# Optimization experiments

Hardware: AMD Instinct MI355X
Metric: run time of the kernel (lower is better)

Reference implementation:

```python
import jax, jax.numpy as jnp
import numpy as np

N_NODES = 100000
N_EDGES = 1600000
NODE_F = 64
EDGE_F = 32
BN_EPS = 1e-5


def setup_inputs() -> dict:
    key = jax.random.key(0)
    ks = jax.random.split(key, 8)
    in_dim = 2 * NODE_F + EDGE_F  # 160
    scale = 1.0 / np.sqrt(in_dim)
    return {
        "node_attrs": jax.random.normal(ks[0], (N_NODES, NODE_F), jnp.float32),
        "edge_index": jax.random.randint(ks[1], (2, N_EDGES), 0, N_NODES, jnp.int64),
        "edge_attrs": jax.random.normal(ks[2], (N_EDGES, EDGE_F), jnp.float32),
        "W_f": jax.random.normal(ks[3], (in_dim, NODE_F), jnp.float32) * scale,
        "b_f": jnp.zeros((NODE_F,), jnp.float32),
        "W_s": jax.random.normal(ks[4], (in_dim, NODE_F), jnp.float32) * scale,
        "b_s": jnp.zeros((NODE_F,), jnp.float32),
        "gamma": jnp.ones((NODE_F,), jnp.float32),
        "beta": jnp.zeros((NODE_F,), jnp.float32),
    }


def reference(node_attrs, edge_index, edge_attrs, W_f, b_f, W_s, b_s, gamma, beta):
    source, target = edge_index[0], edge_index[1]
    x_i = node_attrs[source]            # [E, F] gather
    x_j = node_attrs[target]            # [E, F] gather
    z = jnp.concatenate([x_i, x_j, edge_attrs], axis=-1)  # [E, 2F+Fe]
    # gated MLP: sigmoid(lin_f(z)) * softplus(lin_s(z))
    h = jax.nn.sigmoid(z @ W_f + b_f) * jax.nn.softplus(z @ W_s + b_s)  # [E, F]
    # scatter-add messages to source nodes
    message = jax.ops.segment_sum(h, source, num_segments=node_attrs.shape[0])  # [N, F]
    # BatchNorm1d in training mode: batch stats over node dim (biased variance)
    mean = jnp.mean(message, axis=0)
    var = jnp.mean((message - mean) ** 2, axis=0)
    normed = (message - mean) * jax.lax.rsqrt(var + BN_EPS) * gamma + beta
    return node_attrs + normed
```

## Files before the change

kernel.cpp:

```cpp
#include <hip/hip_runtime.h>
#include <math.h>

#define N_NODES 100000
#define N_EDGES 1600000
#define NODE_F  64
#define IN_DIM  160
#define N_TILES 25000
#define ZSTRIDE 168
#define EDGE_GRID 1536
#define PQ_GRID  2048
#define PRE_GRID 512
#define PRE_TILES 1563

typedef __attribute__((ext_vector_type(8))) short short8;
typedef __attribute__((ext_vector_type(4))) float f32x4;

static __device__ inline unsigned short f2bf(float f) {
    union { float f; unsigned u; } v; v.f = f;
    unsigned r = v.u + 0x7fffu + ((v.u >> 16) & 1u);
    return (unsigned short)(r >> 16);
}

static __device__ inline unsigned pack2(float lo, float hi) {
    union { float f; unsigned u; } a, b; a.f = lo; b.f = hi;
    const unsigned ra = a.u + 0x7fffu + ((a.u >> 16) & 1u);
    const unsigned rb = b.u + 0x7fffu + ((b.u >> 16) & 1u);
    return __builtin_amdgcn_perm(rb, ra, 0x07060302u);
}

__global__ __launch_bounds__(256, 3) void precompute_kernel(
    const float* __restrict__ X,
    const float* __restrict__ W_f, const float* __restrict__ W_s,
    float* __restrict__ PS, float* __restrict__ QT)
{
    __shared__ __align__(16) short wtps[128 * 68];
    __shared__ __align__(16) short wtqt[128 * 68];
    __shared__ __align__(16) short xl[64 * 72];
    unsigned* xl32 = (unsigned*)xl;

    const int tid  = threadIdx.x;
    const int wave = tid >> 6;
    const int lane = tid & 63;
    const int quad = lane >> 4;
    const int l15  = lane & 15;

    for (int idx = tid; idx < 128 * 64; idx += 256) {
        const int c = idx >> 6;
        const int k = idx & 63;
        const int j = c >> 1;
        const float* W = (c & 1) ? W_s : W_f;
        wtps[c * 68 + k] = (short)f2bf(W[k * 64 + j]);
        wtqt[c * 68 + k] = (short)f2bf(W[(k + 64) * 64 + j]);
    }
    __syncthreads();

    const short* wt = (wave >> 1) ? wtqt : wtps;
    const int colbase = (wave & 1) * 64;
    float* const OUT = (wave >> 1) ? QT : PS;

    short8 bfr[4][2];
#pragma unroll
    for (int nt = 0; nt < 4; ++nt)
#pragma unroll
        for (int kc = 0; kc < 2; ++kc)
            bfr[nt][kc] = *(const short8*)&wt[(colbase + nt * 16 + l15) * 68 + kc * 32 + quad * 8];

    for (int t = blockIdx.x; t < PRE_TILES; t += PRE_GRID) {
        const int n0 = t * 64;
        __syncthreads();
        for (int idx = tid; idx < 64 * 16; idx += 256) {
            const int row = idx >> 4, c4 = idx & 15;
            float4 v = {0.f, 0.f, 0.f, 0.f};
            if (n0 + row < N_NODES)
                v = *(const float4*)&X[(size_t)(n0 + row) * 64 + c4 * 4];
            uint2 o; o.x = pack2(v.x, v.y); o.y = pack2(v.z, v.w);
            *(uint2*)&xl32[row * 36 + c4 * 2] = o;
        }
        __syncthreads();

#pragma unroll
        for (int mt = 0; mt < 4; ++mt) {
            short8 a0 = *(const short8*)&xl[(mt * 16 + l15) * 72 + 0 * 32 + quad * 8];
            short8 a1 = *(const short8*)&xl[(mt * 16 + l15) * 72 + 1 * 32 + quad * 8];
#pragma unroll
            for (int nt = 0; nt < 4; ++nt) {
                f32x4 acc = {0.f, 0.f, 0.f, 0.f};
                acc = __builtin_amdgcn_mfma_f32_16x16x32_bf16(a0, bfr[nt][0], acc, 0, 0, 0);
                acc = __builtin_amdgcn_mfma_f32_16x16x32_bf16(a1, bfr[nt][1], acc, 0, 0, 0);
#pragma unroll
                for (int r = 0; r < 4; ++r) {
                    const int node = n0 + mt * 16 + quad * 4 + r;
                    if (node < N_NODES)
                        OUT[(size_t)node * 128 + colbase + nt * 16 + l15] = acc[r];
                }
            }
        }
    }
}

__global__ __launch_bounds__(256, 8) void edge_pq_kernel(
    const float* __restrict__ PS,
    const float* __restrict__ QT,
    const int*   __restrict__ edge_src,
    const int*   __restrict__ edge_tgt,
    const float* __restrict__ edge_attrs,
    const float* __restrict__ W_f, const float* __restrict__ b_f,
    const float* __restrict__ W_s, const float* __restrict__ b_s,
    float* __restrict__ msg)
{
    __shared__ __align__(16) short ebuf[64 * 40];
    __shared__ __align__(16) short wet[64 * 72];

    const int tid  = threadIdx.x;
    const int wave = tid >> 6;
    const int lane = tid & 63;
    const int quad = lane >> 4;
    const int l15  = lane & 15;

    for (int idx = tid; idx < 64 * 32; idx += 256) {
        const int c = idx >> 5, k = idx & 31;
        wet[c * 72 + k]      = (short)f2bf(W_f[(k + 128) * 64 + c]);
        wet[c * 72 + 32 + k] = (short)f2bf(W_s[(k + 128) * 64 + c]);
    }
    __syncthreads();
    const short8 bFe = *(const short8*)&wet[(16 * wave + l15) * 72 + quad * 8];
    const short8 bSe = *(const short8*)&wet[(16 * wave + l15) * 72 + 32 + quad * 8];

    const float bias_f = b_f[16 * wave + l15];
    const float bias_s = b_s[16 * wave + l15];
    const int   fcol2  = 2 * (16 * wave + l15);
    float* const msgf  = msg + 16 * wave + l15;

    const int sel = tid >> 2;
    const int sg  = tid & 3;

    int srcv = edge_src[blockIdx.x * 64 + lane];
    int tgtv = edge_tgt[blockIdx.x * 64 + lane];

    for (int t = blockIdx.x; t < N_TILES; t += PQ_GRID) {
        const int e0 = t * 64;

        __syncthreads();

        {
            const float4 v0 = *(const float4*)&edge_attrs[(size_t)(e0 + sel) * 32 + sg * 8];
            const float4 v1 = *(const float4*)&edge_attrs[(size_t)(e0 + sel) * 32 + sg * 8 + 4];
            short8 o;
            unsigned* o32 = (unsigned*)&o;
            o32[0] = pack2(v0.x, v0.y); o32[1] = pack2(v0.z, v0.w);
            o32[2] = pack2(v1.x, v1.y); o32[3] = pack2(v1.z, v1.w);
            *(short8*)&ebuf[sel * 40 + sg * 8] = o;
        }

        const int tn = t + PQ_GRID;
        int nsrc = 0, ntgt = 0;
        if (tn < N_TILES) {
            nsrc = edge_src[tn * 64 + lane];
            ntgt = edge_tgt[tn * 64 + lane];
        }
        __syncthreads();

#pragma unroll
        for (int mt = 0; mt < 4; ++mt) {
            const short8 a = *(const short8*)&ebuf[(mt * 16 + l15) * 40 + quad * 8];
            f32x4 accF = {0.f, 0.f, 0.f, 0.f};
            f32x4 accS = {0.f, 0.f, 0.f, 0.f};
            accF = __builtin_amdgcn_mfma_f32_16x16x32_bf16(a, bFe, accF, 0, 0, 0);
            accS = __builtin_amdgcn_mfma_f32_16x16x32_bf16(a, bSe, accS, 0, 0, 0);
#pragma unroll
            for (int r = 0; r < 4; ++r) {
                const int e = mt * 16 + quad * 4 + r;
                const int s = __shfl(srcv, e);
                const int g = __shfl(tgtv, e);
                const float2 ps = *(const float2*)&PS[(size_t)s * 128 + fcol2];
                const float2 qt = *(const float2*)&QT[(size_t)g * 128 + fcol2];
                const float xf = accF[r] + ps.x + qt.x + bias_f;
                const float xs = accS[r] + ps.y + qt.y + bias_s;
                const float sig = __builtin_amdgcn_rcpf(1.0f + __expf(-xf));
                const float sp  = fmaxf(xs, 0.0f) + __logf(1.0f + __expf(-fabsf(xs)));
                atomicAdd(&msgf[s * 64], sig * sp);
            }
        }

        srcv = nsrc;
        tgtv = ntgt;
    }
}

__global__ __launch_bounds__(256, 6) void edge_kernel(
    const float* __restrict__ node_attrs,
    const int*   __restrict__ edge_src,
    const int*   __restrict__ edge_tgt,
    const float* __restrict__ edge_attrs,
    const float* __restrict__ W_f, const float* __restrict__ b_f,
    const float* __restrict__ W_s, const float* __restrict__ b_s,
    float* __restrict__ msg)
{
    __shared__ __align__(16) short sbuf[64 * ZSTRIDE];
    unsigned* sbuf32 = (unsigned*)sbuf;

    const int tid  = threadIdx.x;
    const int wave = tid >> 6;
    const int lane = tid & 63;
    const int quad = lane >> 4;
    const int l15  = lane & 15;

    short8 bF[5], bS[5];
#pragma unroll
    for (int mat = 0; mat < 2; ++mat) {
        const float* W = mat ? W_s : W_f;
        __syncthreads();
        for (int idx = tid; idx < IN_DIM * 64; idx += 256) {
            const int k = idx >> 6, n = idx & 63;
            sbuf[n * ZSTRIDE + k] = (short)f2bf(W[idx]);
        }
        __syncthreads();
#pragma unroll
        for (int kc = 0; kc < 5; ++kc) {
            const short8 b = *(const short8*)&sbuf[(16 * wave + l15) * ZSTRIDE + kc * 32 + quad * 8];
            if (mat) bS[kc] = b; else bF[kc] = b;
        }
    }

    const float bias_f = b_f[16 * wave + l15];
    const float bias_s = b_s[16 * wave + l15];
    float* const msgf  = msg + 16 * wave + l15;

    int srcv = edge_src[blockIdx.x * 64 + lane];
    int tgtv = edge_tgt[blockIdx.x * 64 + lane];

    for (int t = blockIdx.x; t < N_TILES; t += EDGE_GRID) {
        const int e0 = t * 64;
        __syncthreads();
#pragma unroll
        for (int i = 0; i < 8; ++i) {
            const int el   = i * 2 + (quad >> 1);
            const int half = quad & 1;
            const int sl   = 16 * wave + el;
            const int ns   = __shfl(srcv, sl);
            const int nt   = __shfl(tgtv, sl);
            const int node = half ? nt : ns;
            const float4 v = *(const float4*)&node_attrs[node * 64 + l15 * 4];
            uint2 o; o.x = pack2(v.x, v.y); o.y = pack2(v.z, v.w);
            *(uint2*)&sbuf32[sl * (ZSTRIDE / 2) + half * 32 + l15 * 2] = o;
        }
#pragma unroll
        for (int i = 0; i < 2; ++i) {
            const int p  = i * 256 + tid;
            const int el = p >> 3, g = p & 7;
            const float4 v = *(const float4*)&edge_attrs[(size_t)(e0 + el) * 32 + g * 4];
            uint2 o; o.x = pack2(v.x, v.y); o.y = pack2(v.z, v.w);
            *(uint2*)&sbuf32[el * (ZSTRIDE / 2) + 64 + g * 2] = o;
        }
        const int tn = t + EDGE_GRID;
        int nsrc = 0, ntgt = 0;
        if (tn < N_TILES) {
            nsrc = edge_src[tn * 64 + lane];
            ntgt = edge_tgt[tn * 64 + lane];
        }
        __syncthreads();
#pragma unroll
        for (int mt = 0; mt < 4; ++mt) {
            f32x4 accF = {0.f, 0.f, 0.f, 0.f};
            f32x4 accS = {0.f, 0.f, 0.f, 0.f};
#pragma unroll
            for (int kc = 0; kc < 5; ++kc) {
                const short8 a = *(const short8*)&sbuf[(mt * 16 + l15) * ZSTRIDE + kc * 32 + quad * 8];
                accF = __builtin_amdgcn_mfma_f32_16x16x32_bf16(a, bF[kc], accF, 0, 0, 0);
                accS = __builtin_amdgcn_mfma_f32_16x16x32_bf16(a, bS[kc], accS, 0, 0, 0);
            }
#pragma unroll
            for (int r = 0; r < 4; ++r) {
                const float xf = accF[r] + bias_f;
                const float xs = accS[r] + bias_s;
                const float sig = __builtin_amdgcn_rcpf(1.0f + __expf(-xf));
                const float sp  = fmaxf(xs, 0.0f) + __logf(1.0f + __expf(-fabsf(xs)));
                const float h   = sig * sp;
                const int sl    = mt * 16 + quad * 4 + r;
                const int node  = __shfl(srcv, sl);
                atomicAdd(&msgf[node * 64], h);
            }
        }
        srcv = nsrc;
        tgtv = ntgt;
    }
}

#define STATS_BLOCKS 400
__global__ __launch_bounds__(256) void stats_kernel(
    const float* __restrict__ msg, float* __restrict__ stats)
{
    const int tid = threadIdx.x;
    const int f = tid & 63;
    const int g = tid >> 6;
    float s = 0.0f, q = 0.0f;
    for (int r = blockIdx.x * 4 + g; r < N_NODES; r += STATS_BLOCKS * 4) {
        const float v = msg[r * 64 + f];
        s += v;
        q = fmaf(v, v, q);
    }
    __shared__ float rs[4][64];
    __shared__ float rq[4][64];
    rs[g][f] = s;
    rq[g][f] = q;
    __syncthreads();
    if (tid < 64) {
        const float ss = rs[0][f] + rs[1][f] + rs[2][f] + rs[3][f];
        const float qq = rq[0][f] + rq[1][f] + rq[2][f] + rq[3][f];
        atomicAdd(&stats[f], ss);
        atomicAdd(&stats[64 + f], qq);
    }
}

__global__ __launch_bounds__(256) void norm_kernel(
    const float* __restrict__ node_attrs,
    const float* __restrict__ stats,
    const float* __restrict__ gamma,
    const float* __restrict__ beta,
    float* __restrict__ out)
{
    const int i = blockIdx.x * blockDim.x + threadIdx.x;
    const int idx = i * 4;
    if (idx >= N_NODES * 64) return;
    const int f = idx & 63;
    const float inv_n = 1.0f / (float)N_NODES;

    const float4 m4 = *(const float4*)&out[idx];
    const float4 x4 = *(const float4*)&node_attrs[idx];

    float mean[4], rstd[4], gm[4], bt[4];
#pragma unroll
    for (int j = 0; j < 4; ++j) {
        mean[j] = stats[f + j] * inv_n;
        const float var = stats[64 + f + j] * inv_n - mean[j] * mean[j];
        rstd[j] = rsqrtf(var + 1e-5f);
        gm[j] = gamma[f + j];
        bt[j] = beta[f + j];
    }
    float4 o;
    o.x = x4.x + (m4.x - mean[0]) * rstd[0] * gm[0] + bt[0];
    o.y = x4.y + (m4.y - mean[1]) * rstd[1] * gm[1] + bt[1];
    o.z = x4.z + (m4.z - mean[2]) * rstd[2] * gm[2] + bt[2];
    o.w = x4.w + (m4.w - mean[3]) * rstd[3] * gm[3] + bt[3];
    *(float4*)&out[idx] = o;
}

extern "C" void kernel_launch(void* const* d_in, const int* in_sizes, int n_in,
                              void* d_out, int out_size, void* d_ws, size_t ws_size,
                              hipStream_t stream)
{
    const float* node_attrs = (const float*)d_in[0];
    const int*   edge_index = (const int*)d_in[1];
    const float* edge_attrs = (const float*)d_in[2];
    const float* W_f   = (const float*)d_in[3];
    const float* b_f   = (const float*)d_in[4];
    const float* W_s   = (const float*)d_in[5];
    const float* b_s   = (const float*)d_in[6];
    const float* gamma = (const float*)d_in[7];
    const float* beta  = (const float*)d_in[8];

    float* out   = (float*)d_out;
    float* stats = (float*)d_ws;

    float* PS = (float*)((char*)d_ws + 4096);
    float* QT = PS + (size_t)N_NODES * 128;
    const size_t WS_NEED = 4096 + 2ull * N_NODES * 128 * sizeof(float);

    const int* edge_src = edge_index;
    const int* edge_tgt = edge_index + N_EDGES;

    hipMemsetAsync(out, 0, (size_t)N_NODES * NODE_F * sizeof(float), stream);
    hipMemsetAsync(stats, 0, 128 * sizeof(float), stream);

    if (ws_size >= WS_NEED) {
        precompute_kernel<<<PRE_GRID, 256, 0, stream>>>(node_attrs, W_f, W_s, PS, QT);
        edge_pq_kernel<<<PQ_GRID, 256, 0, stream>>>(
            PS, QT, edge_src, edge_tgt, edge_attrs, W_f, b_f, W_s, b_s, out);
    } else {
        edge_kernel<<<EDGE_GRID, 256, 0, stream>>>(
            node_attrs, edge_src, edge_tgt, edge_attrs, W_f, b_f, W_s, b_s, out);
    }

    stats_kernel<<<STATS_BLOCKS, 256, 0, stream>>>(out, stats);

    norm_kernel<<<(N_NODES * NODE_F / 4 + 255) / 256, 256, 0, stream>>>(
        node_attrs, stats, gamma, beta, out);
}
```

Measured before the change: 716.2 us.

## Sort edges by source node and aggregate messages per run before atomics

Adds a counting sort of edges by source (histogram, three-stage scan, fill and scatter kernels) so the edge kernel walks edges grouped by source node. Each lane accumulates consecutive same-source contributions in a register and issues one atomic per run, and loads the source's PS row only once per run. The goal is to cut global atomic traffic and redundant PS gathers. In exchange it adds several extra kernel launches with their own atomics and memory passes, and edge_attrs reads become indirect gathers through the permutation.

```diff
diff --git a/kernel.cpp b/kernel.cpp
--- a/kernel.cpp
+++ b/kernel.cpp
@@ -8,9 +8,11 @@
 #define N_TILES 25000
 #define ZSTRIDE 168
 #define EDGE_GRID 1536
-#define PQ_GRID  2048
+#define SPQ_GRID 2048
 #define PRE_GRID 512
 #define PRE_TILES 1563
+#define SCAN_BLOCKS 391
+#define E_BLOCKS    6250
 
 typedef __attribute__((ext_vector_type(8))) short short8;
 typedef __attribute__((ext_vector_type(4))) float f32x4;
@@ -26,6 +28,92 @@
     const unsigned ra = a.u + 0x7fffu + ((a.u >> 16) & 1u);
     const unsigned rb = b.u + 0x7fffu + ((b.u >> 16) & 1u);
     return __builtin_amdgcn_perm(rb, ra, 0x07060302u);
+}
+
+static __device__ inline int permrow(int e) {
+    return ((e >> 2) & 3) * 16 + (e >> 4) * 4 + (e & 3);
+}
+
+__global__ __launch_bounds__(256) void hist_kernel(
+    const int* __restrict__ src, int* __restrict__ hist)
+{
+    const int e = blockIdx.x * 256 + threadIdx.x;
+    if (e < N_EDGES) atomicAdd(&hist[src[e]], 1);
+}
+
+__global__ __launch_bounds__(256) void scan1_kernel(
+    const int* __restrict__ hist, int* __restrict__ partial)
+{
+    __shared__ int lds[256];
+    const int tid = threadIdx.x;
+    const int idx = blockIdx.x * 256 + tid;
+    lds[tid] = (idx < N_NODES) ? hist[idx] : 0;
+    __syncthreads();
+    for (int s = 128; s > 0; s >>= 1) {
+        if (tid < s) lds[tid] += lds[tid + s];
+        __syncthreads();
+    }
+    if (tid == 0) partial[blockIdx.x] = lds[0];
+}
+
+__global__ __launch_bounds__(512) void scan2_kernel(int* __restrict__ partial)
+{
+    __shared__ int lds[512];
+    const int tid = threadIdx.x;
+    const int v = (tid < SCAN_BLOCKS) ? partial[tid] : 0;
+    lds[tid] = v;
+    __syncthreads();
+    for (int off = 1; off < 512; off <<= 1) {
+        const int t = (tid >= off) ? lds[tid - off] : 0;
+        __syncthreads();
+        lds[tid] += t;
+        __syncthreads();
+    }
+    if (tid < SCAN_BLOCKS) partial[tid] = lds[tid] - v;
+}
+
+__global__ __launch_bounds__(256) void scan3_kernel(
+    const int* __restrict__ hist, const int* __restrict__ partial,
+    int* __restrict__ offs, int* __restrict__ cursor)
+{
+    __shared__ int lds[256];
+    const int tid = threadIdx.x;
+    const int idx = blockIdx.x * 256 + tid;
+    const int v = (idx < N_NODES) ? hist[idx] : 0;
+    lds[tid] = v;
+    __syncthreads();
+    for (int off = 1; off < 256; off <<= 1) {
+        const int t = (tid >= off) ? lds[tid - off] : 0;
+        __syncthreads();
+        lds[tid] += t;
+        __syncthreads();
+    }
+    if (idx < N_NODES) {
+        const int x = lds[tid] - v + partial[blockIdx.x];
+        offs[idx]   = x;
+        cursor[idx] = x;
+    }
+}
+
+__global__ __launch_bounds__(256) void fill_src_kernel(
+    const int* __restrict__ offs, int* __restrict__ sSrc)
+{
+    const int n = blockIdx.x * 256 + threadIdx.x;
+    if (n >= N_NODES) return;
+    const int s = offs[n];
+    const int e = (n + 1 < N_NODES) ? offs[n + 1] : N_EDGES;
+    for (int i = s; i < e; ++i) sSrc[i] = n;
+}
+
+__global__ __launch_bounds__(256) void scatter2_kernel(
+    const int* __restrict__ src, const int* __restrict__ tgt,
+    int* __restrict__ cursor, int2* __restrict__ tp)
+{
+    const int e = blockIdx.x * 256 + threadIdx.x;
+    if (e >= N_EDGES) return;
+    const int s = src[e];
+    const int pos = atomicAdd(&cursor[s], 1);
+    tp[pos] = make_int2(tgt[e], e);
 }
 
 __global__ __launch_bounds__(256, 3) void precompute_kernel(
@@ -98,11 +186,11 @@
     }
 }
 
-__global__ __launch_bounds__(256, 8) void edge_pq_kernel(
+__global__ __launch_bounds__(256, 8) void edge_sorted_pq_kernel(
     const float* __restrict__ PS,
     const float* __restrict__ QT,
-    const int*   __restrict__ edge_src,
-    const int*   __restrict__ edge_tgt,
+    const int*   __restrict__ sSrc,
+    const int2*  __restrict__ tp,
     const float* __restrict__ edge_attrs,
     const float* __restrict__ W_f, const float* __restrict__ b_f,
     const float* __restrict__ W_s, const float* __restrict__ b_s,
@@ -134,32 +222,34 @@
     const int sel = tid >> 2;
     const int sg  = tid & 3;
 
-    int srcv = edge_src[blockIdx.x * 64 + lane];
-    int tgtv = edge_tgt[blockIdx.x * 64 + lane];
-
-    for (int t = blockIdx.x; t < N_TILES; t += PQ_GRID) {
-        const int e0 = t * 64;
-
+    int  srcv = sSrc[blockIdx.x * 64 + lane];
+    int2 tpv  = tp[blockIdx.x * 64 + lane];
+
+    for (int t = blockIdx.x; t < N_TILES; t += SPQ_GRID) {
         __syncthreads();
 
         {
-            const float4 v0 = *(const float4*)&edge_attrs[(size_t)(e0 + sel) * 32 + sg * 8];
-            const float4 v1 = *(const float4*)&edge_attrs[(size_t)(e0 + sel) * 32 + sg * 8 + 4];
+            const int pe  = __shfl(tpv.y, sel);
+            const int row = permrow(sel);
+            const float4 v0 = *(const float4*)&edge_attrs[(size_t)pe * 32 + sg * 8];
+            const float4 v1 = *(const float4*)&edge_attrs[(size_t)pe * 32 + sg * 8 + 4];
             short8 o;
             unsigned* o32 = (unsigned*)&o;
             o32[0] = pack2(v0.x, v0.y); o32[1] = pack2(v0.z, v0.w);
             o32[2] = pack2(v1.x, v1.y); o32[3] = pack2(v1.z, v1.w);
-            *(short8*)&ebuf[sel * 40 + sg * 8] = o;
-        }
-
-        const int tn = t + PQ_GRID;
-        int nsrc = 0, ntgt = 0;
+            *(short8*)&ebuf[row * 40 + sg * 8] = o;
+        }
+
+        const int tn = t + SPQ_GRID;
+        int  nsrc = 0; int2 ntp = make_int2(0, 0);
         if (tn < N_TILES) {
-            nsrc = edge_src[tn * 64 + lane];
-            ntgt = edge_tgt[tn * 64 + lane];
-        }
-        __syncthreads();
-
+            nsrc = sSrc[tn * 64 + lane];
+            ntp  = tp[tn * 64 + lane];
+        }
+        __syncthreads();
+
+        int lastn = -1;
+        float carry = 0.0f, psx = 0.0f, psy = 0.0f;
 #pragma unroll
         for (int mt = 0; mt < 4; ++mt) {
             const short8 a = *(const short8*)&ebuf[(mt * 16 + l15) * 40 + quad * 8];
@@ -169,21 +259,27 @@
             accS = __builtin_amdgcn_mfma_f32_16x16x32_bf16(a, bSe, accS, 0, 0, 0);
 #pragma unroll
             for (int r = 0; r < 4; ++r) {
-                const int e = mt * 16 + quad * 4 + r;
-                const int s = __shfl(srcv, e);
-                const int g = __shfl(tgtv, e);
-                const float2 ps = *(const float2*)&PS[(size_t)s * 128 + fcol2];
-                const float2 qt = *(const float2*)&QT[(size_t)g * 128 + fcol2];
-                const float xf = accF[r] + ps.x + qt.x + bias_f;
-                const float xs = accS[r] + ps.y + qt.y + bias_s;
+                const int e = quad * 16 + mt * 4 + r;
+                const int n = __shfl(srcv, e);
+                const int g = __shfl(tpv.x, e);
+                const float2 qt2 = *(const float2*)&QT[(size_t)g * 128 + fcol2];
+                if (n != lastn) {
+                    if (lastn >= 0) atomicAdd(&msgf[lastn * 64], carry);
+                    const float2 p2 = *(const float2*)&PS[(size_t)n * 128 + fcol2];
+                    psx = p2.x; psy = p2.y;
+                    lastn = n; carry = 0.0f;
+                }
+                const float xf = accF[r] + psx + qt2.x + bias_f;
+                const float xs = accS[r] + psy + qt2.y + bias_s;
                 const float sig = __builtin_amdgcn_rcpf(1.0f + __expf(-xf));
                 const float sp  = fmaxf(xs, 0.0f) + __logf(1.0f + __expf(-fabsf(xs)));
-                atomicAdd(&msgf[s * 64], sig * sp);
+                carry += sig * sp;
             }
         }
+        atomicAdd(&msgf[lastn * 64], carry);
 
         srcv = nsrc;
-        tgtv = ntgt;
+        tpv  = ntp;
     }
 }
 
@@ -362,20 +458,34 @@
     float* out   = (float*)d_out;
     float* stats = (float*)d_ws;
 
-    float* PS = (float*)((char*)d_ws + 4096);
-    float* QT = PS + (size_t)N_NODES * 128;
-    const size_t WS_NEED = 4096 + 2ull * N_NODES * 128 * sizeof(float);
+    char* wsb    = (char*)d_ws;
+    int*  partial = (int*)(wsb + 1024);
+    int*  hist    = (int*)(wsb + 4096);
+    int*  offs    = (int*)(wsb + 409600);
+    int*  cursor  = (int*)(wsb + 811008);
+    int*  sSrc    = (int*)(wsb + 1212416);
+    int2* tp      = (int2*)(wsb + 8388608);
+    float* PS     = (float*)(wsb + 25165824);
+    float* QT     = PS + (size_t)N_NODES * 128;
+    const size_t WS_NEED = 25165824 + 2ull * N_NODES * 128 * sizeof(float);
 
     const int* edge_src = edge_index;
     const int* edge_tgt = edge_index + N_EDGES;
 
     hipMemsetAsync(out, 0, (size_t)N_NODES * NODE_F * sizeof(float), stream);
-    hipMemsetAsync(stats, 0, 128 * sizeof(float), stream);
+    hipMemsetAsync(stats, 0, 512, stream);
 
     if (ws_size >= WS_NEED) {
+        hipMemsetAsync(hist, 0, (size_t)N_NODES * sizeof(int), stream);
         precompute_kernel<<<PRE_GRID, 256, 0, stream>>>(node_attrs, W_f, W_s, PS, QT);
-        edge_pq_kernel<<<PQ_GRID, 256, 0, stream>>>(
-            PS, QT, edge_src, edge_tgt, edge_attrs, W_f, b_f, W_s, b_s, out);
+        hist_kernel<<<E_BLOCKS, 256, 0, stream>>>(edge_src, hist);
+        scan1_kernel<<<SCAN_BLOCKS, 256, 0, stream>>>(hist, partial);
+        scan2_kernel<<<1, 512, 0, stream>>>(partial);
+        scan3_kernel<<<SCAN_BLOCKS, 256, 0, stream>>>(hist, partial, offs, cursor);
+        fill_src_kernel<<<SCAN_BLOCKS, 256, 0, stream>>>(offs, sSrc);
+        scatter2_kernel<<<E_BLOCKS, 256, 0, stream>>>(edge_src, edge_tgt, cursor, tp);
+        edge_sorted_pq_kernel<<<SPQ_GRID, 256, 0, stream>>>(
+            PS, QT, sSrc, tp, edge_attrs, W_f, b_f, W_s, b_s, out);
     } else {
         edge_kernel<<<EDGE_GRID, 256, 0, stream>>>(
             node_attrs, edge_src, edge_tgt, edge_attrs, W_f, b_f, W_s, b_s, out);
```

Measured after the change: 726.0 us. About the same (+1.4%).
